# Optimization experiments

Hardware: AMD Instinct MI355X
Metric: run time of the kernel (lower is better)

Reference implementation:

```python
import jax, jax.numpy as jnp
import numpy as np

B, T, N, F_IN = 8, 16, 1000, 16
E = 16000
H, D = 4, 32          # heads, gat_hidden_shape
HL = 64               # lstm hidden
OUT = 8
NEG_SLOPE = 0.2       # PyG GATConv default


def setup_inputs() -> dict:
    key = jax.random.key(0)
    ks = jax.random.split(key, 10)
    def init(k, shape, fan):
        return (jax.random.normal(k, shape, jnp.float32) / np.sqrt(fan)).astype(jnp.float32)
    x = jax.random.normal(ks[0], (B, T, N, F_IN), jnp.float32)
    edge_index = jax.random.randint(ks[1], (2, E), 0, N)
    W_gat = init(ks[2], (F_IN, H * D), F_IN)       # GATConv lin weight
    att_src = init(ks[3], (H, D), D)
    att_dst = init(ks[4], (H, D), D)
    b_gat = jnp.zeros((H * D,), jnp.float32)
    W_ih = init(ks[5], (4 * HL, H * D), H * D)     # LSTM, gate order i,f,g,o
    W_hh = init(ks[6], (4 * HL, HL), HL)
    b_ih = jnp.zeros((4 * HL,), jnp.float32)
    b_hh = jnp.zeros((4 * HL,), jnp.float32)
    W_clf = init(ks[7], (OUT, HL), HL)
    b_clf = jnp.zeros((OUT,), jnp.float32)
    return {"x": x, "edge_index": edge_index, "W_gat": W_gat, "att_src": att_src,
            "att_dst": att_dst, "b_gat": b_gat, "W_ih": W_ih, "W_hh": W_hh,
            "b_ih": b_ih, "b_hh": b_hh, "W_clf": W_clf, "b_clf": b_clf}


def reference(x, edge_index, W_gat, att_src, att_dst, b_gat,
              W_ih, W_hh, b_ih, b_hh, W_clf, b_clf):
    Bx, Tx, Nx, Fx = x.shape
    x_flat = x.reshape(Bx * Tx, Nx, Fx)
    # PyG GATConv adds self-loops by default
    loop = jnp.arange(Nx)
    src = jnp.concatenate([edge_index[0], loop])
    dst = jnp.concatenate([edge_index[1], loop])

    def gat_graph(xg):  # xg: [N, F]
        xp = (xg @ W_gat).reshape(Nx, H, D)                 # [N,H,D]
        a_s = jnp.einsum('nhd,hd->nh', xp, att_src)         # [N,H]
        a_d = jnp.einsum('nhd,hd->nh', xp, att_dst)
        e = jax.nn.leaky_relu(a_s[src] + a_d[dst], NEG_SLOPE)  # [E+N,H]
        m = jax.ops.segment_max(e, dst, num_segments=Nx)       # per-target softmax
        ex = jnp.exp(e - m[dst])
        denom = jax.ops.segment_sum(ex, dst, num_segments=Nx)
        alpha = ex / denom[dst]                                # [E+N,H]
        out = jax.ops.segment_sum(alpha[..., None] * xp[src], dst, num_segments=Nx)
        return out.reshape(Nx, H * D) + b_gat                  # [N, H*D]

    gat = jax.vmap(gat_graph)(x_flat)          # [B*T, N, H*D]
    gat = jax.nn.relu(gat)
    pooled = gat.max(axis=1)                   # global_max_pool -> [B*T, H*D]
    seq = pooled.reshape(Bx, Tx, H * D)

    h0 = jnp.zeros((Bx, HL), jnp.float32)
    c0 = jnp.zeros((Bx, HL), jnp.float32)

    def step(carry, xt):  # xt: [B, H*D]
        h, c = carry
        gates = xt @ W_ih.T + h @ W_hh.T + b_ih + b_hh
        i, f, g, o = jnp.split(gates, 4, axis=-1)
        i, f, o = jax.nn.sigmoid(i), jax.nn.sigmoid(f), jax.nn.sigmoid(o)
        g = jnp.tanh(g)
        c = f * c + i * g
        h = o * jnp.tanh(c)
        return (h, c), None

    (hT, _), _ = jax.lax.scan(step, (h0, c0), seq.transpose(1, 0, 2))
    return hT @ W_clf.T + b_clf                # [B, OUT]
```

## Files before the change

### kernel.cpp

```cpp
#include <hip/hip_runtime.h>
#include <hip/hip_bf16.h>
#include <stdint.h>

namespace {
constexpr int kB = 8, kT = 16, kN = 1000, kF = 16;
constexpr int kE = 16000;
constexpr int kH = 4, kHD = 128;
constexpr int kHL = 64, kOUT = 8;
constexpr int kG = kB * kT;
constexpr float kNeg = 0.2f;
constexpr int kNB = 25;

constexpr size_t CX_WG   = 0;
constexpr size_t CX_ATS  = CX_WG   + 2048;
constexpr size_t CX_ATD  = CX_ATS  + 128;
constexpr size_t CX_BG   = CX_ATD  + 128;
constexpr size_t CX_WIH  = CX_BG   + 128;
constexpr size_t CX_WHH  = CX_WIH  + 32768;
constexpr size_t CX_BIH  = CX_WHH  + 16384;
constexpr size_t CX_BHH  = CX_BIH  + 256;
constexpr size_t CX_WCLF = CX_BHH  + 256;
constexpr size_t CX_BCLF = CX_WCLF + 512;
constexpr size_t CX_TOTAL = CX_BCLF + 8;

constexpr size_t OFF_FLAG  = 0;
constexpr size_t OFF_ROW   = 256;
constexpr size_t OFF_COL   = 4352;
constexpr size_t OFF_POOL  = 68608;
constexpr size_t OFF_CANON = 134400;
constexpr size_t OFF_AS    = 239872;
constexpr size_t OFF_PPART = OFF_AS + (size_t)kG * 288000;
constexpr size_t PPART_BYTES = (size_t)kG * kNB * kHD * 4;

constexpr int kSetupBlocks = 10;
}

__device__ __forceinline__ float bf2f(unsigned short u) {
    return __uint_as_float(((uint32_t)u) << 16);
}
__device__ __forceinline__ float blo(uint32_t u) { return __uint_as_float(u << 16); }
__device__ __forceinline__ unsigned short f2bf(float f) {
    uint32_t u = __float_as_uint(f);
    uint32_t r = (u + 0x7fff + ((u >> 16) & 1)) >> 16;
    return (unsigned short)r;
}
__device__ __forceinline__ float sigm(float x) { return 1.f / (1.f + __expf(-x)); }

__device__ __forceinline__ int detect_isf(const unsigned short* xs, int t,
                                          int nthr, int* sh_cnt) {
    if (t == 0) *sh_cnt = 0;
    __syncthreads();
    int loc = 0;
    for (int i = t; i < 2048; i += nthr) {
        unsigned short u = xs[i];
        int ex = (u >> 7) & 0xff;
        if (u == 0 || (ex >= 97 && ex <= 143)) loc++;
    }
    atomicAdd(sh_cnt, loc);
    __syncthreads();
    return (*sh_cnt >= (2048 * 8) / 10) ? 0 : 1;
}

struct ConvArgs {
    const unsigned short* src[10];
    int n[10];
};

__global__ __launch_bounds__(256) void mega_setup(
        const void* __restrict__ xraw, const int* __restrict__ ei,
        ConvArgs ca,
        const unsigned short* __restrict__ WgR,
        const unsigned short* __restrict__ atsR,
        const unsigned short* __restrict__ atdR,
        int* __restrict__ flag, int* __restrict__ row, int* __restrict__ col,
        unsigned short* __restrict__ canon,
        unsigned short* __restrict__ xp_all,
        float* __restrict__ as_all, float* __restrict__ ad_all,
        unsigned int* __restrict__ pooled) {
    const int t = threadIdx.x;
    const unsigned short* xs = (const unsigned short*)xraw;

    if (blockIdx.x == 0) {
        __shared__ int cnt[1024];
        __shared__ int wtot[4];
        const int lane = t & 63, w = t >> 6;
        for (int i = t; i < 1024; i += 256) cnt[i] = 0;
        __syncthreads();
        const int* dst = ei + kE;
        for (int e = t; e < kE; e += 256) atomicAdd(&cnt[dst[e]], 1);
        __syncthreads();
        const int n0 = 4 * t;
        int c0 = cnt[n0], c1 = cnt[n0 + 1], c2 = cnt[n0 + 2], c3 = cnt[n0 + 3];
        int s0 = c0, s1 = s0 + c1, s2 = s1 + c2, s3 = s2 + c3;
        int tot = s3;
#pragma unroll
        for (int sft = 1; sft < 64; sft <<= 1) {
            int v = __shfl_up(tot, sft, 64);
            if (lane >= sft) tot += v;
        }
        if (lane == 63) wtot[w] = tot;
        __syncthreads();
        int wexcl = 0;
        for (int j = 0; j < w; ++j) wexcl += wtot[j];
        const int excl = wexcl + tot - s3;
        if (t == 0) row[0] = 0;
        if (n0 < kN) {
            row[n0 + 1] = excl + s0;
            row[n0 + 2] = excl + s1;
            row[n0 + 3] = excl + s2;
            row[n0 + 4] = excl + s3;
        }
        __syncthreads();
        cnt[n0] = excl; cnt[n0 + 1] = excl + s0;
        cnt[n0 + 2] = excl + s1; cnt[n0 + 3] = excl + s2;
        __syncthreads();
        for (int e = t; e < kE; e += 256) {
            int d0 = dst[e];
            int pos = atomicAdd(&cnt[d0], 1);
            col[pos] = ei[e];
        }
    } else if (blockIdx.x <= 8) {
        __shared__ int dcnt;
        const int isf = detect_isf(xs, t, 256, &dcnt);
        if (blockIdx.x == 1 && t == 0) *flag = isf;
        const int gid = (int)(blockIdx.x - 1) * 256 + t;
        size_t base = 0;
        for (int s = 0; s < 10; ++s) {
            const int n = ca.n[s];
            if (isf) {
                const float* fp = (const float*)ca.src[s];
                for (int i = gid; i < n; i += 2048) canon[base + i] = f2bf(fp[i]);
            } else {
                const unsigned short* sp = ca.src[s];
                for (int i = gid; i < n; i += 2048) canon[base + i] = sp[i];
            }
            base += (size_t)n;
        }
    } else if (blockIdx.x == 9) {
        for (int i = t; i < kG * kHD; i += 256) pooled[i] = 0u;
    } else {
        __shared__ int dcnt;
        __shared__ float Wl[kF * kHD];
        __shared__ float asl[kHD], adl[kHD];
        __shared__ float xr[64][20];
        __shared__ float ws2[2][4][16];
        const int isf = detect_isf(xs, t, 256, &dcnt);
        const int i0 = blockIdx.x - kSetupBlocks;
        const int v = i0 & 7;
        const int jj = i0 >> 3;
        const int gl = v + 8 * (jj >> 4);
        const int nb = jj & 15;
        if (isf) {
            const float* wf = (const float*)WgR;
            for (int i = t; i < kF * kHD; i += 256) Wl[i] = wf[i];
            if (t < kHD) asl[t] = ((const float*)atsR)[t];
            else if (t < 2 * kHD) adl[t - kHD] = ((const float*)atdR)[t - kHD];
        } else {
            for (int i = t; i < kF * kHD; i += 256) Wl[i] = bf2f(WgR[i]);
            if (t < kHD) asl[t] = bf2f(atsR[t]);
            else if (t < 2 * kHD) adl[t - kHD] = bf2f(atdR[t - kHD]);
        }
        const int n0 = nb * 64;
        const int nn = min(64, kN - n0);
        const size_t xbase = (size_t)gl * kN * kF + (size_t)n0 * kF;
        if (isf) {
            const float* xf = (const float*)xraw;
            for (int i = t; i < nn * kF; i += 256) xr[i >> 4][i & 15] = xf[xbase + i];
        } else {
            for (int i = t; i < nn * kF; i += 256) xr[i >> 4][i & 15] = bf2f(xs[xbase + i]);
        }
        __syncthreads();

        if (t < 128) {
            const int sd = t >> 6, h = (t >> 4) & 3, f = t & 15;
            const float* att = sd ? adl : asl;
            const int d0r = t & 31;
            float acc = 0.f;
#pragma unroll
            for (int i = 0; i < 32; ++i) {
                const int d = (d0r + i) & 31;
                acc += Wl[f * kHD + h * 32 + d] * att[h * 32 + d];
            }
            ws2[sd][h][f] = acc;
        }

        uint32_t* xp32 = (uint32_t*)(xp_all + (size_t)gl * kN * kHD);
        {
            const int p = t & 63;
            const int q = t >> 6;
            const int c0 = 2 * p;
            float wA[kF], wB[kF];
#pragma unroll
            for (int f = 0; f < kF; ++f) {
                wA[f] = Wl[f * kHD + c0];
                wB[f] = Wl[f * kHD + c0 + 1];
            }
            for (int ln = q; ln < nn; ln += 4) {
                const float4* xrv = (const float4*)xr[ln];
                const float4 x0 = xrv[0], x1 = xrv[1], x2 = xrv[2], x3 = xrv[3];
                float vA = x0.x * wA[0]  + x0.y * wA[1]  + x0.z * wA[2]  + x0.w * wA[3]
                         + x1.x * wA[4]  + x1.y * wA[5]  + x1.z * wA[6]  + x1.w * wA[7]
                         + x2.x * wA[8]  + x2.y * wA[9]  + x2.z * wA[10] + x2.w * wA[11]
                         + x3.x * wA[12] + x3.y * wA[13] + x3.z * wA[14] + x3.w * wA[15];
                float vB = x0.x * wB[0]  + x0.y * wB[1]  + x0.z * wB[2]  + x0.w * wB[3]
                         + x1.x * wB[4]  + x1.y * wB[5]  + x1.z * wB[6]  + x1.w * wB[7]
                         + x2.x * wB[8]  + x2.y * wB[9]  + x2.z * wB[10] + x2.w * wB[11]
                         + x3.x * wB[12] + x3.y * wB[13] + x3.z * wB[14] + x3.w * wB[15];
                const uint32_t pk = (uint32_t)f2bf(vA) | ((uint32_t)f2bf(vB) << 16);
                xp32[(size_t)(n0 + ln) * 64 + p] = pk;
            }
        }
        __syncthreads();

        {
            const int n = t >> 2, h = t & 3;
            if (n < nn) {
                const float* xv = xr[n];
                const float* wsv = ws2[0][h];
                const float* wdv = ws2[1][h];
                float accS = 0.f, accD = 0.f;
#pragma unroll
                for (int f = 0; f < kF; ++f) {
                    const float xf = xv[f];
                    accS += xf * wsv[f];
                    accD += xf * wdv[f];
                }
                as_all[((size_t)gl * kN + n0 + n) * kH + h] = accS;
                ad_all[((size_t)gl * kN + n0 + n) * kH + h] = accD;
            }
        }
    }
}

__global__ __launch_bounds__(256) void gat_aggregate(
        const int* __restrict__ row, const int* __restrict__ col,
        const unsigned short* __restrict__ xp,
        const float* __restrict__ a_s, const float* __restrict__ a_d,
        const unsigned short* __restrict__ bg,
        unsigned int* __restrict__ pooled,
        float* __restrict__ part, int use_part) {
    __shared__ int   col_lds[4][64];
    __shared__ float p_lds[4][4][72];
    __shared__ float pm[4][kHD];

    const int w = threadIdx.x >> 6;
    const int lane = threadIdx.x & 63;
    const int sub = lane >> 4;
    const int cl = lane & 15;
    const int hh = cl >> 2;
    const int xcd = blockIdx.x & 7;
    const int j = blockIdx.x >> 3;
    const int gl = xcd + 8 * (j / kNB);
    const int blk = j % kNB;
    const size_t gn = (size_t)gl * kN;
    const char* xpcl = (const char*)(xp + gn * kHD) + cl * 16;
    const float4* as4 = (const float4*)a_s + gn;
    const float4* ad4 = (const float4*)a_d + gn;
    const uint32_t* bg32 = (const uint32_t*)bg;
    float bgv[8];
#pragma unroll
    for (int jb = 0; jb < 4; ++jb) {
        uint32_t u = bg32[cl * 4 + jb];
        bgv[2 * jb] = blo(u);
        bgv[2 * jb + 1] = __uint_as_float(u & 0xffff0000u);
    }
    float pool[8];
#pragma unroll
    for (int jb = 0; jb < 8; ++jb) pool[jb] = 0.f;

    for (int it = 0; it < 10; ++it) {
        const int n = blk * 40 + it * 4 + w;
        const int r0 = row[n];
        const int deg = row[n + 1] - r0;
        const int E = deg + 1;
        const float4 dv = ad4[n];
        float acc[8];
#pragma unroll
        for (int jb = 0; jb < 8; ++jb) acc[jb] = 0.f;
        float dh = 0.f;

        for (int base = 0; base < E; base += 64) {
            const int cnt = min(64, E - base);
            const int cntP = (cnt + 3) & ~3;
            if (lane < cntP) {
                const int eg = base + lane;
                const bool act = lane < cnt;
                const int s = (act && eg < deg) ? col[r0 + eg] : n;
                float p0 = 0.f, p1 = 0.f, p2 = 0.f, p3 = 0.f;
                if (act) {
                    const float4 av = as4[s];
                    float t0 = av.x + dv.x, t1 = av.y + dv.y;
                    float t2 = av.z + dv.z, t3 = av.w + dv.w;
                    t0 = t0 > 0.f ? t0 : kNeg * t0;
                    t1 = t1 > 0.f ? t1 : kNeg * t1;
                    t2 = t2 > 0.f ? t2 : kNeg * t2;
                    t3 = t3 > 0.f ? t3 : kNeg * t3;
                    p0 = __expf(t0); p1 = __expf(t1);
                    p2 = __expf(t2); p3 = __expf(t3);
                }
                col_lds[w][lane] = s << 8;
                p_lds[w][0][lane] = p0;
                p_lds[w][1][lane] = p1;
                p_lds[w][2][lane] = p2;
                p_lds[w][3][lane] = p3;
            }
            for (int e0 = 0; e0 < cntP; e0 += 4) {
                const int e = e0 + sub;
                const int off = col_lds[w][e];
                const float al = p_lds[w][hh][e];
                const uint4 u = *(const uint4*)(xpcl + off);
                acc[0] += al * blo(u.x); acc[1] += al * __uint_as_float(u.x);
                acc[2] += al * blo(u.y); acc[3] += al * __uint_as_float(u.y);
                acc[4] += al * blo(u.z); acc[5] += al * __uint_as_float(u.z);
                acc[6] += al * blo(u.w); acc[7] += al * __uint_as_float(u.w);
                dh += al;
            }
        }
#pragma unroll
        for (int jb = 0; jb < 8; ++jb) {
            acc[jb] += __shfl_xor(acc[jb], 16, 64);
            acc[jb] += __shfl_xor(acc[jb], 32, 64);
        }
        dh += __shfl_xor(dh, 16, 64);
        dh += __shfl_xor(dh, 32, 64);
        const float inv = 1.f / dh;
#pragma unroll
        for (int jb = 0; jb < 8; ++jb) {
            const float o = acc[jb] * inv + bgv[jb];
            pool[jb] = fmaxf(pool[jb], o > 0.f ? o : 0.f);
        }
    }
    if (sub == 0) {
#pragma unroll
        for (int jb = 0; jb < 8; ++jb) pm[w][cl * 8 + jb] = pool[jb];
    }
    __syncthreads();
    if (w == 0 && sub == 0) {
        if (use_part) {
            float* dst = part + ((size_t)gl * kNB + blk) * kHD;
#pragma unroll
            for (int jb = 0; jb < 8; ++jb) {
                const int c = cl * 8 + jb;
                dst[c] = fmaxf(fmaxf(pm[0][c], pm[1][c]), fmaxf(pm[2][c], pm[3][c]));
            }
        } else {
            const size_t gp = (size_t)gl * kHD;
#pragma unroll
            for (int jb = 0; jb < 8; ++jb) {
                const int c = cl * 8 + jb;
                float vmax = fmaxf(fmaxf(pm[0][c], pm[1][c]), fmaxf(pm[2][c], pm[3][c]));
                atomicMax(pooled + gp + c, __float_as_uint(vmax));
            }
        }
    }
}

__global__ __launch_bounds__(256) void lstm_head(
        const float* __restrict__ pooled, const float* __restrict__ part,
        int use_part,
        const unsigned short* __restrict__ Wih,
        const unsigned short* __restrict__ Whh,
        const unsigned short* __restrict__ bih,
        const unsigned short* __restrict__ bhh,
        const unsigned short* __restrict__ Wclf,
        const unsigned short* __restrict__ bclf,
        const int* __restrict__ flag,
        void* __restrict__ out) {
    const int b = blockIdx.x;
    const int r = threadIdx.x;
    __shared__ float xt[kHD];
    __shared__ float hs[kHL];
    __shared__ float gates[4 * kHL];

    uint32_t wih[64];
    const uint32_t* pw = (const uint32_t*)(Wih + (size_t)r * kHD);
#pragma unroll
    for (int j = 0; j < 64; ++j) wih[j] = pw[j];
    uint32_t whh[32];
    const uint32_t* ph = (const uint32_t*)(Whh + (size_t)r * kHL);
#pragma unroll
    for (int j = 0; j < 32; ++j) whh[j] = ph[j];
    const float bias = bf2f(bih[r]) + bf2f(bhh[r]);

    float c_st = 0.f;
    if (r < kHL) hs[r] = 0.f;
    __syncthreads();

    for (int t = 0; t < kT; ++t) {
        const size_t g = (size_t)b * kT + t;
        if (r < kHD) {
            if (use_part) {
                const float* ps = part + g * kNB * kHD + r;
                float v = ps[0];
#pragma unroll
                for (int k = 1; k < kNB; ++k) v = fmaxf(v, ps[(size_t)k * kHD]);
                xt[r] = v;
            } else {
                xt[r] = pooled[g * kHD + r];
            }
        }
        __syncthreads();
        float a0 = 0.f, a1 = 0.f, a2 = 0.f, a3 = 0.f;
#pragma unroll
        for (int j = 0; j < 64; j += 4) {
            uint32_t u0 = wih[j], u1 = wih[j + 1], u2 = wih[j + 2], u3 = wih[j + 3];
            a0 += blo(u0) * xt[2 * j + 0] + __uint_as_float(u0 & 0xffff0000u) * xt[2 * j + 1];
            a1 += blo(u1) * xt[2 * j + 2] + __uint_as_float(u1 & 0xffff0000u) * xt[2 * j + 3];
            a2 += blo(u2) * xt[2 * j + 4] + __uint_as_float(u2 & 0xffff0000u) * xt[2 * j + 5];
            a3 += blo(u3) * xt[2 * j + 6] + __uint_as_float(u3 & 0xffff0000u) * xt[2 * j + 7];
        }
#pragma unroll
        for (int j = 0; j < 32; j += 4) {
            uint32_t u0 = whh[j], u1 = whh[j + 1], u2 = whh[j + 2], u3 = whh[j + 3];
            a0 += blo(u0) * hs[2 * j + 0] + __uint_as_float(u0 & 0xffff0000u) * hs[2 * j + 1];
            a1 += blo(u1) * hs[2 * j + 2] + __uint_as_float(u1 & 0xffff0000u) * hs[2 * j + 3];
            a2 += blo(u2) * hs[2 * j + 4] + __uint_as_float(u2 & 0xffff0000u) * hs[2 * j + 5];
            a3 += blo(u3) * hs[2 * j + 6] + __uint_as_float(u3 & 0xffff0000u) * hs[2 * j + 7];
        }
        gates[r] = bias + (a0 + a1) + (a2 + a3);
        __syncthreads();
        if (r < kHL) {
            const float iv = sigm(gates[r]);
            const float fv = sigm(gates[kHL + r]);
            const float gv = tanhf(gates[2 * kHL + r]);
            const float ov = sigm(gates[3 * kHL + r]);
            c_st = fv * c_st + iv * gv;
            hs[r] = ov * tanhf(c_st);
        }
        __syncthreads();
    }
    if (r < kOUT) {
        float acc = bf2f(bclf[r]);
#pragma unroll
        for (int k = 0; k < kHL; ++k) acc += hs[k] * bf2f(Wclf[r * kHL + k]);
        if (*flag) ((float*)out)[b * kOUT + r] = acc;
        else ((__hip_bfloat16*)out)[b * kOUT + r] = __float2bfloat16(acc);
    }
}

extern "C" void kernel_launch(void* const* d_in, const int* in_sizes, int n_in,
                              void* d_out, int out_size, void* d_ws, size_t ws_size,
                              hipStream_t stream) {
    const int* ei = (const int*)d_in[1];

    char* ws = (char*)d_ws;
    int*            flag   = (int*)(ws + OFF_FLAG);
    int*            row    = (int*)(ws + OFF_ROW);
    int*            colv   = (int*)(ws + OFF_COL);
    unsigned int*   pooled = (unsigned int*)(ws + OFF_POOL);
    unsigned short* canon  = (unsigned short*)(ws + OFF_CANON);

    unsigned short* cBg   = canon + CX_BG;
    unsigned short* cWih  = canon + CX_WIH;
    unsigned short* cWhh  = canon + CX_WHH;
    unsigned short* cBih  = canon + CX_BIH;
    unsigned short* cBhh  = canon + CX_BHH;
    unsigned short* cWclf = canon + CX_WCLF;
    unsigned short* cBclf = canon + CX_BCLF;

    float*          a_s = (float*)(ws + OFF_AS);
    float*          a_d = (float*)(ws + OFF_AS + (size_t)kG * 16000);
    unsigned short* xp  = (unsigned short*)(ws + OFF_AS + (size_t)kG * 32000);

    const int use_part = (ws_size >= OFF_PPART + PPART_BYTES) ? 1 : 0;
    float* part = (float*)(ws + OFF_PPART);

    ConvArgs ca;
    const int sizes[10] = {2048, 128, 128, 128, 32768, 16384, 256, 256, 512, 8};
    const int which[10] = {2, 3, 4, 5, 6, 7, 8, 9, 10, 11};
    for (int i = 0; i < 10; ++i) {
        ca.src[i] = (const unsigned short*)d_in[which[i]];
        ca.n[i] = sizes[i];
    }

    mega_setup<<<kSetupBlocks + kG * 16, 256, 0, stream>>>(
        d_in[0], ei, ca,
        (const unsigned short*)d_in[2], (const unsigned short*)d_in[3],
        (const unsigned short*)d_in[4],
        flag, row, colv, canon, xp, a_s, a_d, pooled);
    gat_aggregate<<<kG * kNB, 256, 0, stream>>>(row, colv, xp, a_s, a_d, cBg,
                                                pooled, part, use_part);
    lstm_head<<<kB, 256, 0, stream>>>((const float*)pooled, part, use_part,
                                      cWih, cWhh, cBih, cBhh,
                                      cWclf, cBclf, flag, d_out);
}
```

Before: 221.3 us.

## Move partial max-pool reduction into aggregate tail; halve setup blocks with packed weights

The last block per graph in gat_aggregate, found through a global atomic counter, now reduces the per-block partial max-pool results, so lstm_head no longer does a serial 25-way reduction on each timestep. The setup kernel detects the input dtype with a single-wave shuffle reduction instead of shared atomics and barriers. Each projection block now handles two 64-node tiles with packed bf16 weights held in registers, so the block count drops by half. In exchange the change adds a threadfence/atomic handoff and rounds the GAT weights to bf16 even when the input is fp32.

```diff
diff --git a/kernel.cpp b/kernel.cpp
--- a/kernel.cpp
+++ b/kernel.cpp
@@ -31,6 +31,7 @@
 constexpr size_t OFF_AS    = 239872;
 constexpr size_t OFF_PPART = OFF_AS + (size_t)kG * 288000;
 constexpr size_t PPART_BYTES = (size_t)kG * kNB * kHD * 4;
+constexpr size_t OFF_CNTG  = OFF_PPART + PPART_BYTES;
 
 constexpr int kSetupBlocks = 10;
 }
@@ -39,6 +40,7 @@
     return __uint_as_float(((uint32_t)u) << 16);
 }
 __device__ __forceinline__ float blo(uint32_t u) { return __uint_as_float(u << 16); }
+__device__ __forceinline__ float bhx(uint32_t u) { return __uint_as_float(u & 0xffff0000u); }
 __device__ __forceinline__ unsigned short f2bf(float f) {
     uint32_t u = __float_as_uint(f);
     uint32_t r = (u + 0x7fff + ((u >> 16) & 1)) >> 16;
@@ -46,19 +48,21 @@
 }
 __device__ __forceinline__ float sigm(float x) { return 1.f / (1.f + __expf(-x)); }
 
-__device__ __forceinline__ int detect_isf(const unsigned short* xs, int t,
-                                          int nthr, int* sh_cnt) {
-    if (t == 0) *sh_cnt = 0;
-    __syncthreads();
+__device__ __forceinline__ int detect_isf_wave(const uint32_t* __restrict__ x32) {
+    const int lane = threadIdx.x & 63;
     int loc = 0;
-    for (int i = t; i < 2048; i += nthr) {
-        unsigned short u = xs[i];
-        int ex = (u >> 7) & 0xff;
-        if (u == 0 || (ex >= 97 && ex <= 143)) loc++;
-    }
-    atomicAdd(sh_cnt, loc);
-    __syncthreads();
-    return (*sh_cnt >= (2048 * 8) / 10) ? 0 : 1;
+#pragma unroll
+    for (int r = 0; r < 8; ++r) {
+        const uint32_t u = x32[r * 64 + lane];
+        const unsigned short a = (unsigned short)(u & 0xffffu);
+        const unsigned short b = (unsigned short)(u >> 16);
+        const int ea = (a >> 7) & 0xff, eb = (b >> 7) & 0xff;
+        loc += (a == 0 || (ea >= 97 && ea <= 143)) ? 1 : 0;
+        loc += (b == 0 || (eb >= 97 && eb <= 143)) ? 1 : 0;
+    }
+#pragma unroll
+    for (int s = 1; s < 64; s <<= 1) loc += __shfl_xor(loc, s, 64);
+    return (loc >= 820) ? 0 : 1;
 }
 
 struct ConvArgs {
@@ -76,9 +80,10 @@
         unsigned short* __restrict__ canon,
         unsigned short* __restrict__ xp_all,
         float* __restrict__ as_all, float* __restrict__ ad_all,
-        unsigned int* __restrict__ pooled) {
+        unsigned int* __restrict__ pooled, int* __restrict__ cnt_g) {
     const int t = threadIdx.x;
     const unsigned short* xs = (const unsigned short*)xraw;
+    const uint32_t* x32 = (const uint32_t*)xraw;
 
     if (blockIdx.x == 0) {
         __shared__ int cnt[1024];
@@ -120,8 +125,7 @@
             col[pos] = ei[e];
         }
     } else if (blockIdx.x <= 8) {
-        __shared__ int dcnt;
-        const int isf = detect_isf(xs, t, 256, &dcnt);
+        const int isf = detect_isf_wave(x32);
         if (blockIdx.x == 1 && t == 0) *flag = isf;
         const int gid = (int)(blockIdx.x - 1) * 256 + t;
         size_t base = 0;
@@ -138,38 +142,37 @@
         }
     } else if (blockIdx.x == 9) {
         for (int i = t; i < kG * kHD; i += 256) pooled[i] = 0u;
+        if (t < kG) cnt_g[t] = 0;
     } else {
-        __shared__ int dcnt;
-        __shared__ float Wl[kF * kHD];
+        __shared__ uint32_t Wl32[kF * 64];
         __shared__ float asl[kHD], adl[kHD];
         __shared__ float xr[64][20];
         __shared__ float ws2[2][4][16];
-        const int isf = detect_isf(xs, t, 256, &dcnt);
+        const int isf = detect_isf_wave(x32);
         const int i0 = blockIdx.x - kSetupBlocks;
         const int v = i0 & 7;
         const int jj = i0 >> 3;
-        const int gl = v + 8 * (jj >> 4);
-        const int nb = jj & 15;
+        const int gl = v + 8 * (jj >> 3);
+        const int pairIdx = jj & 7;
         if (isf) {
             const float* wf = (const float*)WgR;
-            for (int i = t; i < kF * kHD; i += 256) Wl[i] = wf[i];
+            for (int i = t; i < kF * 64; i += 256)
+                Wl32[i] = (uint32_t)f2bf(wf[2 * i]) | ((uint32_t)f2bf(wf[2 * i + 1]) << 16);
             if (t < kHD) asl[t] = ((const float*)atsR)[t];
             else if (t < 2 * kHD) adl[t - kHD] = ((const float*)atdR)[t - kHD];
         } else {
-            for (int i = t; i < kF * kHD; i += 256) Wl[i] = bf2f(WgR[i]);
+            const uint32_t* w32 = (const uint32_t*)WgR;
+            for (int i = t; i < kF * 64; i += 256) Wl32[i] = w32[i];
             if (t < kHD) asl[t] = bf2f(atsR[t]);
             else if (t < 2 * kHD) adl[t - kHD] = bf2f(atdR[t - kHD]);
         }
-        const int n0 = nb * 64;
-        const int nn = min(64, kN - n0);
-        const size_t xbase = (size_t)gl * kN * kF + (size_t)n0 * kF;
-        if (isf) {
-            const float* xf = (const float*)xraw;
-            for (int i = t; i < nn * kF; i += 256) xr[i >> 4][i & 15] = xf[xbase + i];
-        } else {
-            for (int i = t; i < nn * kF; i += 256) xr[i >> 4][i & 15] = bf2f(xs[xbase + i]);
-        }
-        __syncthreads();
+        __syncthreads();
+
+        const int p = t & 63;
+        const int q = t >> 6;
+        uint32_t wP[kF];
+#pragma unroll
+        for (int f = 0; f < kF; ++f) wP[f] = Wl32[f * 64 + p];
 
         if (t < 128) {
             const int sd = t >> 6, h = (t >> 4) & 3, f = t & 15;
@@ -179,54 +182,65 @@
 #pragma unroll
             for (int i = 0; i < 32; ++i) {
                 const int d = (d0r + i) & 31;
-                acc += Wl[f * kHD + h * 32 + d] * att[h * 32 + d];
+                const uint32_t u = Wl32[f * 64 + h * 16 + (d >> 1)];
+                const float wv = (d & 1) ? bhx(u) : blo(u);
+                acc += wv * att[h * 32 + d];
             }
             ws2[sd][h][f] = acc;
         }
 
         uint32_t* xp32 = (uint32_t*)(xp_all + (size_t)gl * kN * kHD);
-        {
-            const int p = t & 63;
-            const int q = t >> 6;
-            const int c0 = 2 * p;
-            float wA[kF], wB[kF];
-#pragma unroll
-            for (int f = 0; f < kF; ++f) {
-                wA[f] = Wl[f * kHD + c0];
-                wB[f] = Wl[f * kHD + c0 + 1];
-            }
+        for (int tt = 0; tt < 2; ++tt) {
+            const int nb = pairIdx * 2 + tt;
+            const int n0 = nb * 64;
+            const int nn = min(64, kN - n0);
+            __syncthreads();
+            const size_t xbase = (size_t)gl * kN * kF + (size_t)n0 * kF;
+            if (isf) {
+                const float* xf = (const float*)xraw;
+                for (int i = t; i < nn * kF; i += 256) xr[i >> 4][i & 15] = xf[xbase + i];
+            } else {
+                const uint32_t* xv32 = (const uint32_t*)(xs + xbase);
+                for (int i2 = t; i2 < nn * 8; i2 += 256) {
+                    const uint32_t u = xv32[i2];
+                    const int n = i2 >> 3, f2 = (i2 & 7) * 2;
+                    xr[n][f2] = blo(u);
+                    xr[n][f2 + 1] = bhx(u);
+                }
+            }
+            __syncthreads();
+
             for (int ln = q; ln < nn; ln += 4) {
                 const float4* xrv = (const float4*)xr[ln];
                 const float4 x0 = xrv[0], x1 = xrv[1], x2 = xrv[2], x3 = xrv[3];
-                float vA = x0.x * wA[0]  + x0.y * wA[1]  + x0.z * wA[2]  + x0.w * wA[3]
-                         + x1.x * wA[4]  + x1.y * wA[5]  + x1.z * wA[6]  + x1.w * wA[7]
-                         + x2.x * wA[8]  + x2.y * wA[9]  + x2.z * wA[10] + x2.w * wA[11]
-                         + x3.x * wA[12] + x3.y * wA[13] + x3.z * wA[14] + x3.w * wA[15];
-                float vB = x0.x * wB[0]  + x0.y * wB[1]  + x0.z * wB[2]  + x0.w * wB[3]
-                         + x1.x * wB[4]  + x1.y * wB[5]  + x1.z * wB[6]  + x1.w * wB[7]
-                         + x2.x * wB[8]  + x2.y * wB[9]  + x2.z * wB[10] + x2.w * wB[11]
-                         + x3.x * wB[12] + x3.y * wB[13] + x3.z * wB[14] + x3.w * wB[15];
+                float vA = 0.f, vB = 0.f;
+                const float xf_[kF] = {x0.x, x0.y, x0.z, x0.w, x1.x, x1.y, x1.z, x1.w,
+                                       x2.x, x2.y, x2.z, x2.w, x3.x, x3.y, x3.z, x3.w};
+#pragma unroll
+                for (int f = 0; f < kF; ++f) {
+                    vA += xf_[f] * blo(wP[f]);
+                    vB += xf_[f] * bhx(wP[f]);
+                }
                 const uint32_t pk = (uint32_t)f2bf(vA) | ((uint32_t)f2bf(vB) << 16);
                 xp32[(size_t)(n0 + ln) * 64 + p] = pk;
             }
-        }
-        __syncthreads();
-
-        {
-            const int n = t >> 2, h = t & 3;
-            if (n < nn) {
-                const float* xv = xr[n];
-                const float* wsv = ws2[0][h];
-                const float* wdv = ws2[1][h];
-                float accS = 0.f, accD = 0.f;
-#pragma unroll
-                for (int f = 0; f < kF; ++f) {
-                    const float xf = xv[f];
-                    accS += xf * wsv[f];
-                    accD += xf * wdv[f];
+
+            {
+                const int n = t >> 2, h = t & 3;
+                if (n < nn) {
+                    const float* xv = xr[n];
+                    const float* wsv = ws2[0][h];
+                    const float* wdv = ws2[1][h];
+                    float accS = 0.f, accD = 0.f;
+#pragma unroll
+                    for (int f = 0; f < kF; ++f) {
+                        const float xf = xv[f];
+                        accS += xf * wsv[f];
+                        accD += xf * wdv[f];
+                    }
+                    as_all[((size_t)gl * kN + n0 + n) * kH + h] = accS;
+                    ad_all[((size_t)gl * kN + n0 + n) * kH + h] = accD;
                 }
-                as_all[((size_t)gl * kN + n0 + n) * kH + h] = accS;
-                ad_all[((size_t)gl * kN + n0 + n) * kH + h] = accD;
             }
         }
     }
@@ -238,10 +252,11 @@
         const float* __restrict__ a_s, const float* __restrict__ a_d,
         const unsigned short* __restrict__ bg,
         unsigned int* __restrict__ pooled,
-        float* __restrict__ part, int use_part) {
+        float* __restrict__ part, int* __restrict__ cnt_g, int use_part) {
     __shared__ int   col_lds[4][64];
     __shared__ float p_lds[4][4][72];
     __shared__ float pm[4][kHD];
+    __shared__ int   sh_last;
 
     const int w = threadIdx.x >> 6;
     const int lane = threadIdx.x & 63;
@@ -262,7 +277,7 @@
     for (int jb = 0; jb < 4; ++jb) {
         uint32_t u = bg32[cl * 4 + jb];
         bgv[2 * jb] = blo(u);
-        bgv[2 * jb + 1] = __uint_as_float(u & 0xffff0000u);
+        bgv[2 * jb + 1] = bhx(u);
     }
     float pool[8];
 #pragma unroll
@@ -353,11 +368,27 @@
             }
         }
     }
+    if (use_part) {
+        __threadfence();
+        __syncthreads();
+        if (threadIdx.x == 0)
+            sh_last = (atomicAdd(&cnt_g[gl], 1) == kNB - 1) ? 1 : 0;
+        __syncthreads();
+        if (sh_last) {
+            __threadfence();
+            for (int c = threadIdx.x; c < kHD; c += 256) {
+                const float* ps = part + (size_t)gl * kNB * kHD + c;
+                float vv = ps[0];
+#pragma unroll
+                for (int k = 1; k < kNB; ++k) vv = fmaxf(vv, ps[(size_t)k * kHD]);
+                ((float*)pooled)[(size_t)gl * kHD + c] = vv;
+            }
+        }
+    }
 }
 
 __global__ __launch_bounds__(256) void lstm_head(
-        const float* __restrict__ pooled, const float* __restrict__ part,
-        int use_part,
+        const float* __restrict__ pooled,
         const unsigned short* __restrict__ Wih,
         const unsigned short* __restrict__ Whh,
         const unsigned short* __restrict__ bih,
@@ -387,35 +418,24 @@
     __syncthreads();
 
     for (int t = 0; t < kT; ++t) {
-        const size_t g = (size_t)b * kT + t;
-        if (r < kHD) {
-            if (use_part) {
-                const float* ps = part + g * kNB * kHD + r;
-                float v = ps[0];
-#pragma unroll
-                for (int k = 1; k < kNB; ++k) v = fmaxf(v, ps[(size_t)k * kHD]);
-                xt[r] = v;
-            } else {
-                xt[r] = pooled[g * kHD + r];
-            }
-        }
+        if (r < kHD) xt[r] = pooled[((size_t)b * kT + t) * kHD + r];
         __syncthreads();
         float a0 = 0.f, a1 = 0.f, a2 = 0.f, a3 = 0.f;
 #pragma unroll
         for (int j = 0; j < 64; j += 4) {
             uint32_t u0 = wih[j], u1 = wih[j + 1], u2 = wih[j + 2], u3 = wih[j + 3];
-            a0 += blo(u0) * xt[2 * j + 0] + __uint_as_float(u0 & 0xffff0000u) * xt[2 * j + 1];
-            a1 += blo(u1) * xt[2 * j + 2] + __uint_as_float(u1 & 0xffff0000u) * xt[2 * j + 3];
-            a2 += blo(u2) * xt[2 * j + 4] + __uint_as_float(u2 & 0xffff0000u) * xt[2 * j + 5];
-            a3 += blo(u3) * xt[2 * j + 6] + __uint_as_float(u3 & 0xffff0000u) * xt[2 * j + 7];
+            a0 += blo(u0) * xt[2 * j + 0] + bhx(u0) * xt[2 * j + 1];
+            a1 += blo(u1) * xt[2 * j + 2] + bhx(u1) * xt[2 * j + 3];
+            a2 += blo(u2) * xt[2 * j + 4] + bhx(u2) * xt[2 * j + 5];
+            a3 += blo(u3) * xt[2 * j + 6] + bhx(u3) * xt[2 * j + 7];
         }
 #pragma unroll
         for (int j = 0; j < 32; j += 4) {
             uint32_t u0 = whh[j], u1 = whh[j + 1], u2 = whh[j + 2], u3 = whh[j + 3];
-            a0 += blo(u0) * hs[2 * j + 0] + __uint_as_float(u0 & 0xffff0000u) * hs[2 * j + 1];
-            a1 += blo(u1) * hs[2 * j + 2] + __uint_as_float(u1 & 0xffff0000u) * hs[2 * j + 3];
-            a2 += blo(u2) * hs[2 * j + 4] + __uint_as_float(u2 & 0xffff0000u) * hs[2 * j + 5];
-            a3 += blo(u3) * hs[2 * j + 6] + __uint_as_float(u3 & 0xffff0000u) * hs[2 * j + 7];
+            a0 += blo(u0) * hs[2 * j + 0] + bhx(u0) * hs[2 * j + 1];
+            a1 += blo(u1) * hs[2 * j + 2] + bhx(u1) * hs[2 * j + 3];
+            a2 += blo(u2) * hs[2 * j + 4] + bhx(u2) * hs[2 * j + 5];
+            a3 += blo(u3) * hs[2 * j + 6] + bhx(u3) * hs[2 * j + 7];
         }
         gates[r] = bias + (a0 + a1) + (a2 + a3);
         __syncthreads();
@@ -462,8 +482,9 @@
     float*          a_d = (float*)(ws + OFF_AS + (size_t)kG * 16000);
     unsigned short* xp  = (unsigned short*)(ws + OFF_AS + (size_t)kG * 32000);
 
-    const int use_part = (ws_size >= OFF_PPART + PPART_BYTES) ? 1 : 0;
-    float* part = (float*)(ws + OFF_PPART);
+    const int use_part = (ws_size >= OFF_CNTG + (size_t)kG * 4) ? 1 : 0;
+    float* part  = (float*)(ws + OFF_PPART);
+    int*   cnt_g = (int*)(ws + OFF_CNTG);
 
     ConvArgs ca;
     const int sizes[10] = {2048, 128, 128, 128, 32768, 16384, 256, 256, 512, 8};
@@ -473,14 +494,14 @@
         ca.n[i] = sizes[i];
     }
 
-    mega_setup<<<kSetupBlocks + kG * 16, 256, 0, stream>>>(
+    mega_setup<<<kSetupBlocks + kG * 8, 256, 0, stream>>>(
         d_in[0], ei, ca,
         (const unsigned short*)d_in[2], (const unsigned short*)d_in[3],
         (const unsigned short*)d_in[4],
-        flag, row, colv, canon, xp, a_s, a_d, pooled);
+        flag, row, colv, canon, xp, a_s, a_d, pooled, cnt_g);
     gat_aggregate<<<kG * kNB, 256, 0, stream>>>(row, colv, xp, a_s, a_d, cBg,
-                                                pooled, part, use_part);
-    lstm_head<<<kB, 256, 0, stream>>>((const float*)pooled, part, use_part,
+                                                pooled, part, cnt_g, use_part);
+    lstm_head<<<kB, 256, 0, stream>>>((const float*)pooled,
                                       cWih, cWhh, cBih, cBhh,
                                       cWclf, cBclf, flag, d_out);
 }
```

After: 463.3 us. 109% more time.
